# Performance work log

Measured on AMD Instinct MI355X. Metric: run time of the kernel, lower is better.

## Reference

```python
import jax, jax.numpy as jnp
import numpy as np
import math

D_MODEL = 1024
N_HEADS = 16
HEAD_DIM = D_MODEL // N_HEADS
B, S = 2, 2048


def setup_inputs() -> dict:
    key = jax.random.key(0)
    ks = jax.random.split(key, 12)
    sd = 1.0 / math.sqrt(D_MODEL)
    inp = {
        "x": jax.random.normal(ks[0], (B, S, D_MODEL), dtype=jnp.float32),
        "time_gaps": jax.random.uniform(ks[1], (B, S, 1), dtype=jnp.float32),
        "mask": jnp.ones((B, S), dtype=jnp.int32),
        "Wq": jax.random.normal(ks[2], (D_MODEL, D_MODEL), dtype=jnp.float32) * sd,
        "bq": jnp.zeros((D_MODEL,), dtype=jnp.float32),
        "Wk": jax.random.normal(ks[3], (D_MODEL, D_MODEL), dtype=jnp.float32) * sd,
        "bk": jnp.zeros((D_MODEL,), dtype=jnp.float32),
        "Wv": jax.random.normal(ks[4], (D_MODEL, D_MODEL), dtype=jnp.float32) * sd,
        "bv": jnp.zeros((D_MODEL,), dtype=jnp.float32),
        "Wo": jax.random.normal(ks[5], (D_MODEL, D_MODEL), dtype=jnp.float32) * sd,
        "bo": jnp.zeros((D_MODEL,), dtype=jnp.float32),
        "Wt": jax.random.normal(ks[6], (D_MODEL, 1), dtype=jnp.float32),
        "bt": jnp.zeros((D_MODEL,), dtype=jnp.float32),
    }
    return inp


def reference(x, time_gaps, mask, Wq, bq, Wk, bk, Wv, bv, Wo, bo, Wt, bt):
    Bb, Ss, _ = x.shape
    # time embedding: Linear(1, d_model)
    time_emb = time_gaps @ Wt.T + bt            # [B,S,D]
    x_time = x + time_emb

    def split_heads(t):
        return t.reshape(Bb, Ss, N_HEADS, HEAD_DIM).transpose(0, 2, 1, 3)  # [B,H,S,d]

    q = split_heads(x_time @ Wq.T + bq)
    k = split_heads(x_time @ Wk.T + bk)
    v = split_heads(x @ Wv.T + bv)

    scores = jnp.einsum('bhqd,bhkd->bhqk', q, k) / math.sqrt(HEAD_DIM)
    # padding mask: mask==0 positions set to -1e9 (mask broadcast as [B,1,1,S])
    pad = (mask == 0)[:, None, None, :]
    scores = jnp.where(pad, -1e9, scores)
    # causal mask
    causal = jnp.triu(jnp.ones((Ss, Ss), dtype=bool), k=1)
    scores = jnp.where(causal, -1e9, scores)

    attn = jax.nn.softmax(scores, axis=-1)      # dropout is identity in eval
    out = jnp.einsum('bhqk,bhkd->bhqd', attn, v)
    out = out.transpose(0, 2, 1, 3).reshape(Bb, Ss, D_MODEL)
    return out @ Wo.T + bo
```

## Files before the change

### kernel.cpp

```cpp
#include <hip/hip_runtime.h>

typedef short v8s __attribute__((ext_vector_type(8)));
typedef short v4s __attribute__((ext_vector_type(4)));
typedef float v4f __attribute__((ext_vector_type(4)));
typedef int   v4i __attribute__((ext_vector_type(4)));

constexpr int Bb = 2, S = 2048, D = 1024, H = 16;
constexpr int M = Bb * S;

#define DEV __device__ __forceinline__

DEV short f2bf(float f){
  unsigned u = __builtin_bit_cast(unsigned, f);
  u = (u + 0x7FFF + ((u >> 16) & 1)) >> 16;
  return (short)u;
}

DEV int swz(int r){ return (r ^ (r >> 2)) & 7; }

DEV int cvtpk(float lo, float hi){
  int r;
  asm("v_cvt_pk_bf16_f32 %0, %1, %2" : "=v"(r) : "v"(lo), "v"(hi));
  return r;
}

DEV float max3f(float a, float b, float c){
  float r;
  asm("v_max3_f32 %0, %1, %2, %3" : "=v"(r) : "v"(a), "v"(b), "v"(c));
  return r;
}

#define EXP2 exp2f

#define GLDS(gp, lp) __builtin_amdgcn_global_load_lds( \
    (const __attribute__((address_space(1))) void*)(gp), \
    (__attribute__((address_space(3))) void*)(lp), 16, 0, 0)

struct PrepArgs {
  const float* x; const float* tg; const float* Wt; const float* bt;
  const float* Ws0; const float* Ws1; const float* Ws2; const float* Ws3;
  short* Wd0; short* Wd1; short* Wd2; short* Wd3;
  short* xb; short* xtb;
};
__global__ void prep_all(PrepArgs a){
  const int bx = blockIdx.x;
  if (bx < 4096){
    int i = bx * 256 + threadIdx.x;
    int row = i >> 8;
    int c4  = i & 255;
    float4 xv = reinterpret_cast<const float4*>(a.x)[i];
    float4 wv = reinterpret_cast<const float4*>(a.Wt)[c4];
    float4 bv = reinterpret_cast<const float4*>(a.bt)[c4];
    float g = a.tg[row];
    float xs[4] = {xv.x, xv.y, xv.z, xv.w};
    float ws[4] = {wv.x, wv.y, wv.z, wv.w};
    float bs[4] = {bv.x, bv.y, bv.z, bv.w};
    v4s p, q;
    #pragma unroll
    for (int e = 0; e < 4; ++e){
      p[e] = f2bf(xs[e]);
      q[e] = f2bf(xs[e] + g * ws[e] + bs[e]);
    }
    *reinterpret_cast<v4s*>(&a.xb[(size_t)i * 4])  = p;
    *reinterpret_cast<v4s*>(&a.xtb[(size_t)i * 4]) = q;
  } else {
    const int bi = bx - 4096;
    const int widx = bi >> 10;
    const float* src = widx == 0 ? a.Ws0 : widx == 1 ? a.Ws1 : widx == 2 ? a.Ws2 : a.Ws3;
    short* dst = widx == 0 ? a.Wd0 : widx == 1 ? a.Wd1 : widx == 2 ? a.Wd2 : a.Wd3;
    int i = (bi & 1023) * 256 + threadIdx.x;
    float4 v = reinterpret_cast<const float4*>(src)[i];
    v4s o; o[0] = f2bf(v.x); o[1] = f2bf(v.y); o[2] = f2bf(v.z); o[3] = f2bf(v.w);
    *reinterpret_cast<v4s*>(&dst[(size_t)i * 4]) = o;
  }
}

template<int MODE>
DEV void gemm_core(const short* __restrict__ A, const short* __restrict__ Bw,
                   const float* __restrict__ bias, float alpha, void* __restrict__ Cout,
                   int ldc, int m0, int n0){
  __shared__ short As[2][128 * 64];
  __shared__ short Bs[2][128 * 64];
  const int t = threadIdx.x;
  const int w = t >> 6, l = t & 63;
  const int wm = (w >> 1) * 64, wn = (w & 1) * 64;

  v4f acc[4][4] = {};

  auto stage = [&](int kt, int buf){
    const int k0 = kt * 64;
    #pragma unroll
    for (int j = 0; j < 4; ++j){
      const int cix = j * 256 + t;
      const int row = cix >> 3;
      const int c   = (cix & 7) ^ swz(row);
      GLDS(A  + (size_t)(m0 + row) * D + k0 + c * 8, &As[buf][cix * 8]);
      GLDS(Bw + (size_t)(n0 + row) * D + k0 + c * 8, &Bs[buf][cix * 8]);
    }
  };

  stage(0, 0);
  for (int kt = 0; kt < 16; ++kt){
    const int cur = kt & 1;
    __syncthreads();
    if (kt < 15) stage(kt + 1, cur ^ 1);
    #pragma unroll
    for (int kk = 0; kk < 2; ++kk){
      v8s af[4], bfr[4];
      #pragma unroll
      for (int mi = 0; mi < 4; ++mi){
        const int R = wm + mi * 16 + (l & 15);
        af[mi] = *reinterpret_cast<const v8s*>(&As[cur][R * 64 + (((kk * 4 + (l >> 4)) ^ swz(R)) * 8)]);
      }
      #pragma unroll
      for (int ni = 0; ni < 4; ++ni){
        const int R = wn + ni * 16 + (l & 15);
        bfr[ni] = *reinterpret_cast<const v8s*>(&Bs[cur][R * 64 + (((kk * 4 + (l >> 4)) ^ swz(R)) * 8)]);
      }
      __builtin_amdgcn_s_setprio(1);
      #pragma unroll
      for (int mi = 0; mi < 4; ++mi)
        #pragma unroll
        for (int ni = 0; ni < 4; ++ni)
          acc[mi][ni] = __builtin_amdgcn_mfma_f32_16x16x32_bf16(af[mi], bfr[ni], acc[mi][ni], 0, 0, 0);
      __builtin_amdgcn_s_setprio(0);
    }
  }

  #pragma unroll
  for (int mi = 0; mi < 4; ++mi){
    const int row = m0 + wm + mi * 16 + (l >> 4) * 4;
    #pragma unroll
    for (int ni = 0; ni < 4; ++ni){
      const int col = n0 + wn + ni * 16 + (l & 15);
      const float bcol = (MODE == 1) ? 0.f : bias[col];
      #pragma unroll
      for (int r = 0; r < 4; ++r){
        float bsel = (MODE == 1) ? bias[row + r] : bcol;
        float val = (acc[mi][ni][r] + bsel) * alpha;
        if (MODE == 2) reinterpret_cast<float*>(Cout)[(size_t)(row + r) * ldc + col] = val;
        else           reinterpret_cast<short*>(Cout)[(size_t)(row + r) * ldc + col] = f2bf(val);
      }
    }
  }
}

template<int MODE>
__global__ __launch_bounds__(256, 2)
void gemm_bt(const short* __restrict__ A, const short* __restrict__ Bw,
             const float* __restrict__ bias, float alpha, void* __restrict__ Cout, int ldc){
  gemm_core<MODE>(A, Bw, bias, alpha, Cout, ldc, blockIdx.x * 128, blockIdx.y * 128);
}

__global__ __launch_bounds__(256, 2)
void gemm_qk(const short* __restrict__ A, const short* __restrict__ Wq,
             const short* __restrict__ Wk, const float* __restrict__ bq,
             const float* __restrict__ bk, float qalpha,
             short* __restrict__ Qb, short* __restrict__ Kb){
  const bool isK = blockIdx.y >= 8;
  gemm_core<0>(A, isK ? Wk : Wq, isK ? bk : bq, isK ? 1.0f : qalpha,
               isK ? (void*)Kb : (void*)Qb, D, blockIdx.x * 128, (blockIdx.y & 7) * 128);
}

__global__ __launch_bounds__(256, 3)
void attn_kernel(const short* __restrict__ Q, const short* __restrict__ K,
                 const short* __restrict__ VT, const int* __restrict__ maskp,
                 short* __restrict__ O){
  __shared__ short Ks[3][64 * 64];
  __shared__ short Vs[3][64 * 64];
  __shared__ int mflag;
  const int t = threadIdx.x, w = t >> 6, l = t & 63;
  const int g = l >> 4, q16 = l & 15;
  const int bh = blockIdx.x, b = bh >> 4, h = bh & 15;
  const int qx = 31 - (int)blockIdx.y;
  const int q0 = qx * 64;
  const int qw = q0 + w * 16;
  const int qg = qw + q16;
  const int nkt = qx + 1;

  if (t == 0) mflag = 1;
  __syncthreads();
  {
    bool ok = true;
    const int tot = nkt * 64;
    for (int i = t * 4; i < tot; i += 1024){
      v4i mm = *reinterpret_cast<const v4i*>(&maskp[b * S + i]);
      ok = ok && (mm[0] != 0) && (mm[1] != 0) && (mm[2] != 0) && (mm[3] != 0);
    }
    if (!__all(ok)) mflag = 0;
  }
  __syncthreads();
  const bool ALLV = (mflag != 0);

  v8s qf[2];
  #pragma unroll
  for (int kc = 0; kc < 2; ++kc)
    qf[kc] = *reinterpret_cast<const v8s*>(
        &Q[(size_t)(b * S + qg) * D + h * 64 + kc * 32 + g * 8]);

  int kOff[4][2], vOff[4][2];
  #pragma unroll
  for (int nt = 0; nt < 4; ++nt){
    const int R = 32 * (nt >> 1) + 8 * (q16 >> 2) + 4 * (nt & 1) + (l & 3);
    #pragma unroll
    for (int kc = 0; kc < 2; ++kc)
      kOff[nt][kc] = R * 64 + (((kc * 4 + g) ^ swz(R)) * 8);
  }
  #pragma unroll
  for (int dt = 0; dt < 4; ++dt){
    const int R = dt * 16 + q16;
    #pragma unroll
    for (int kc = 0; kc < 2; ++kc)
      vOff[dt][kc] = R * 64 + (((kc * 4 + g) ^ swz(R)) * 8);
  }

  v4f accOT[4] = {};
  v4f accL = {};
  float mrow = -1e30f;

  const v4i onesW = {0x3F803F80, 0x3F803F80, 0x3F803F80, 0x3F803F80};
  const v8s onesv = __builtin_bit_cast(v8s, onesW);

  auto stage = [&](int kt){
    const int buf = kt % 3;
    const int kv0 = kt * 64;
    #pragma unroll
    for (int j = 0; j < 2; ++j){
      const int cix = j * 256 + t;
      const int row = cix >> 3;
      const int c   = (cix & 7) ^ swz(row);
      GLDS(K  + (size_t)(b * S + kv0 + row) * D + h * 64 + c * 8, &Ks[buf][cix * 8]);
      GLDS(VT + (size_t)(h * 64 + row) * M + b * S + kv0 + c * 8, &Vs[buf][cix * 8]);
    }
  };

  auto softmax_pv = [&](float (&p)[16], const short* vb){
    float t0 = max3f(p[0], p[1], p[2]);
    float t1 = max3f(p[3], p[4], p[5]);
    float t2 = max3f(p[6], p[7], p[8]);
    float t3 = max3f(p[9], p[10], p[11]);
    float t4 = max3f(p[12], p[13], p[14]);
    float tm = max3f(max3f(t0, t1, t2), t3, fmaxf(t4, p[15]));
    if (!__all(tm <= mrow + 8.0f)){
      float tmax = fmaxf(tm, __shfl_xor(tm, 16));
      tmax = fmaxf(tmax, __shfl_xor(tmax, 32));
      const float mnew = fmaxf(mrow, tmax);
      const float resc = EXP2(mrow - mnew);
      #pragma unroll
      for (int dt = 0; dt < 4; ++dt) accOT[dt] *= resc;
      accL *= resc;
      mrow = mnew;
    }
    #pragma unroll
    for (int j = 0; j < 16; ++j) p[j] = EXP2(p[j] - mrow);

    int pb[2][4];
    #pragma unroll
    for (int kc = 0; kc < 2; ++kc)
      #pragma unroll
      for (int s = 0; s < 4; ++s){
        const int base = (2 * kc + (s >> 1)) * 4 + (s & 1) * 2;
        pb[kc][s] = cvtpk(p[base], p[base + 1]);
      }

    __builtin_amdgcn_s_setprio(1);
    #pragma unroll
    for (int kc = 0; kc < 2; ++kc){
      v4i tmp = {pb[kc][0], pb[kc][1], pb[kc][2], pb[kc][3]};
      v8s pbv = __builtin_bit_cast(v8s, tmp);
      accL = __builtin_amdgcn_mfma_f32_16x16x32_bf16(onesv, pbv, accL, 0, 0, 0);
      #pragma unroll
      for (int dt = 0; dt < 4; ++dt){
        v8s vf = *reinterpret_cast<const v8s*>(vb + vOff[dt][kc]);
        accOT[dt] = __builtin_amdgcn_mfma_f32_16x16x32_bf16(vf, pbv, accOT[dt], 0, 0, 0);
      }
    }
    __builtin_amdgcn_s_setprio(0);
  };

  auto qk = [&](const short* kb, v4f (&sc)[4]){
    __builtin_amdgcn_s_setprio(1);
    #pragma unroll
    for (int nt = 0; nt < 4; ++nt)
      #pragma unroll
      for (int kc = 0; kc < 2; ++kc){
        v8s kf = *reinterpret_cast<const v8s*>(kb + kOff[nt][kc]);
        sc[nt] = __builtin_amdgcn_mfma_f32_16x16x32_bf16(kf, qf[kc], sc[nt], 0, 0, 0);
      }
    __builtin_amdgcn_s_setprio(0);
  };

  stage(0);
  if (nkt > 1) stage(1);

  if (ALLV){
    for (int kt = 0; kt < nkt; ++kt){
      if (kt + 1 < nkt) asm volatile("s_waitcnt vmcnt(4)" ::: "memory");
      else              asm volatile("s_waitcnt vmcnt(0)" ::: "memory");
      __builtin_amdgcn_s_barrier();
      if (kt + 2 < nkt) stage(kt + 2);

      const int buf = kt % 3;
      const short* kb = Ks[buf];
      const short* vb = Vs[buf];

      v4f sc[4] = {};
      qk(kb, sc);

      float p[16];
      if (kt < qx){
        #pragma unroll
        for (int j = 0; j < 16; ++j) p[j] = sc[j >> 2][j & 3];
      } else {
        const int kv0 = kt * 64;
        #pragma unroll
        for (int nt = 0; nt < 4; ++nt)
          #pragma unroll
          for (int r = 0; r < 4; ++r){
            const int kvg = kv0 + 32 * (nt >> 1) + 8 * g + 4 * (nt & 1) + r;
            p[nt * 4 + r] = (kvg > qg) ? -1e30f : sc[nt][r];
          }
      }
      softmax_pv(p, vb);
    }
  } else {
    for (int kt = 0; kt < nkt; ++kt){
      asm volatile("s_waitcnt vmcnt(0)" ::: "memory");
      __builtin_amdgcn_s_barrier();
      if (kt + 2 < nkt) stage(kt + 2);

      const int buf = kt % 3;
      const short* kb = Ks[buf];
      const short* vb = Vs[buf];
      const int kv0 = kt * 64;

      v4i mq[4];
      #pragma unroll
      for (int nt = 0; nt < 4; ++nt)
        mq[nt] = *reinterpret_cast<const v4i*>(
            &maskp[b * S + kv0 + 32 * (nt >> 1) + 8 * g + 4 * (nt & 1)]);

      v4f sc[4] = {};
      qk(kb, sc);

      float p[16];
      #pragma unroll
      for (int nt = 0; nt < 4; ++nt)
        #pragma unroll
        for (int r = 0; r < 4; ++r){
          const int kvg = kv0 + 32 * (nt >> 1) + 8 * g + 4 * (nt & 1) + r;
          const int kvx = (mq[nt][r] != 0) ? kvg : 0x7fffffff;
          p[nt * 4 + r] = (kvx > qg) ? -1e30f : sc[nt][r];
        }
      softmax_pv(p, vb);
    }
  }

  const float inv = 1.0f / accL[0];
  #pragma unroll
  for (int dt = 0; dt < 4; ++dt){
    v4s o4;
    #pragma unroll
    for (int r = 0; r < 4; ++r) o4[r] = f2bf(accOT[dt][r] * inv);
    *reinterpret_cast<v4s*>(
        &O[(size_t)(b * S + qg) * D + h * 64 + dt * 16 + g * 4]) = o4;
  }
}

extern "C" void kernel_launch(void* const* d_in, const int* in_sizes, int n_in,
                              void* d_out, int out_size, void* d_ws, size_t ws_size,
                              hipStream_t stream){
  const float* x   = (const float*)d_in[0];
  const float* tg  = (const float*)d_in[1];
  const int*   msk = (const int*)d_in[2];
  const float* Wq  = (const float*)d_in[3];
  const float* bq  = (const float*)d_in[4];
  const float* Wk  = (const float*)d_in[5];
  const float* bk  = (const float*)d_in[6];
  const float* Wv  = (const float*)d_in[7];
  const float* bv  = (const float*)d_in[8];
  const float* Wo  = (const float*)d_in[9];
  const float* bo  = (const float*)d_in[10];
  const float* Wt  = (const float*)d_in[11];
  const float* bt  = (const float*)d_in[12];

  char* ws = (char*)d_ws;
  const size_t MB = 1u << 20;
  short* xb  = (short*)(ws);
  short* xtb = (short*)(ws + 8 * MB);
  short* Wqb = (short*)(ws + 16 * MB);
  short* Wkb = (short*)(ws + 18 * MB);
  short* Wvb = (short*)(ws + 20 * MB);
  short* Wob = (short*)(ws + 22 * MB);
  short* Qb  = (short*)(ws + 24 * MB);
  short* Kb  = (short*)(ws + 32 * MB);
  short* VTb = (short*)(ws + 40 * MB);
  short* Ab  = (short*)(ws + 48 * MB);

  PrepArgs pa;
  pa.x = x; pa.tg = tg; pa.Wt = Wt; pa.bt = bt;
  pa.Ws0 = Wq; pa.Ws1 = Wk; pa.Ws2 = Wv; pa.Ws3 = Wo;
  pa.Wd0 = Wqb; pa.Wd1 = Wkb; pa.Wd2 = Wvb; pa.Wd3 = Wob;
  pa.xb = xb; pa.xtb = xtb;
  prep_all<<<8192, 256, 0, stream>>>(pa);

  const float qalpha = 0.125f * 1.4426950408889634f;
  gemm_qk<<<dim3(M / 128, 16), 256, 0, stream>>>(xtb, Wqb, Wkb, bq, bk, qalpha, Qb, Kb);
  gemm_bt<1><<<dim3(D / 128, M / 128), 256, 0, stream>>>(Wvb, xb, bv, 1.0f, VTb, M);

  attn_kernel<<<dim3(Bb * H, 32), 256, 0, stream>>>(Qb, Kb, VTb, msk, Ab);

  gemm_bt<2><<<dim3(M / 128, D / 128), 256, 0, stream>>>(Ab, Wob, bo, 1.0f, (float*)d_out, D);
}
```

Baseline: 117.4 us.

## Fuse Q/K/V projections into one launch and double-buffer attention for occupancy

Merges the QK projection GEMM and the transposed V projection GEMM into a single 768-block launch, removing one kernel launch and the tail between them. The attention kernel drops from triple to double buffering of K/V tiles, which cuts LDS use so launch bounds can rise to 4 blocks per CU. It also remaps query-block order so heavy and light causal tiles interleave. The cost is a shallower prefetch: every iteration now waits for all outstanding loads, so global-load latency is hidden less.

```diff
diff --git a/kernel.cpp b/kernel.cpp
--- a/kernel.cpp
+++ b/kernel.cpp
@@ -153,26 +153,37 @@
 }
 
 __global__ __launch_bounds__(256, 2)
-void gemm_qk(const short* __restrict__ A, const short* __restrict__ Wq,
-             const short* __restrict__ Wk, const float* __restrict__ bq,
-             const float* __restrict__ bk, float qalpha,
-             short* __restrict__ Qb, short* __restrict__ Kb){
-  const bool isK = blockIdx.y >= 8;
-  gemm_core<0>(A, isK ? Wk : Wq, isK ? bk : bq, isK ? 1.0f : qalpha,
-               isK ? (void*)Kb : (void*)Qb, D, blockIdx.x * 128, (blockIdx.y & 7) * 128);
-}
-
-__global__ __launch_bounds__(256, 3)
+void gemm_qkv(const short* __restrict__ xtb, const short* __restrict__ xb,
+              const short* __restrict__ Wqb, const short* __restrict__ Wkb,
+              const short* __restrict__ Wvb,
+              const float* __restrict__ bq, const float* __restrict__ bk,
+              const float* __restrict__ bv, float qalpha,
+              short* __restrict__ Qb, short* __restrict__ Kb, short* __restrict__ VTb){
+  const int id = blockIdx.x;
+  if (id < 512){
+    const int li = id;
+    const int yq = li >> 5;
+    const bool isK = yq >= 8;
+    gemm_core<0>(xtb, isK ? Wkb : Wqb, isK ? bk : bq, isK ? 1.0f : qalpha,
+                 isK ? (void*)Kb : (void*)Qb, D, (li & 31) * 128, (yq & 7) * 128);
+  } else {
+    const int li = id - 512;
+    gemm_core<1>(Wvb, xb, bv, 1.0f, VTb, M, (li & 7) * 128, (li >> 3) * 128);
+  }
+}
+
+__global__ __launch_bounds__(256, 4)
 void attn_kernel(const short* __restrict__ Q, const short* __restrict__ K,
                  const short* __restrict__ VT, const int* __restrict__ maskp,
                  short* __restrict__ O){
-  __shared__ short Ks[3][64 * 64];
-  __shared__ short Vs[3][64 * 64];
+  __shared__ short Ks[2][64 * 64];
+  __shared__ short Vs[2][64 * 64];
   __shared__ int mflag;
   const int t = threadIdx.x, w = t >> 6, l = t & 63;
   const int g = l >> 4, q16 = l & 15;
   const int bh = blockIdx.x, b = bh >> 4, h = bh & 15;
-  const int qx = 31 - (int)blockIdx.y;
+  const int yy = (int)blockIdx.y;
+  const int qx = (yy < 8) ? 31 - yy : (yy < 16) ? yy - 8 : (yy < 24) ? 39 - yy : yy - 16;
   const int q0 = qx * 64;
   const int qw = q0 + w * 16;
   const int qg = qw + q16;
@@ -222,7 +233,7 @@
   const v8s onesv = __builtin_bit_cast(v8s, onesW);
 
   auto stage = [&](int kt){
-    const int buf = kt % 3;
+    const int buf = kt & 1;
     const int kv0 = kt * 64;
     #pragma unroll
     for (int j = 0; j < 2; ++j){
@@ -291,18 +302,15 @@
   };
 
   stage(0);
-  if (nkt > 1) stage(1);
 
   if (ALLV){
     for (int kt = 0; kt < nkt; ++kt){
-      if (kt + 1 < nkt) asm volatile("s_waitcnt vmcnt(4)" ::: "memory");
-      else              asm volatile("s_waitcnt vmcnt(0)" ::: "memory");
+      asm volatile("s_waitcnt vmcnt(0)" ::: "memory");
       __builtin_amdgcn_s_barrier();
-      if (kt + 2 < nkt) stage(kt + 2);
-
-      const int buf = kt % 3;
-      const short* kb = Ks[buf];
-      const short* vb = Vs[buf];
+      if (kt + 1 < nkt) stage(kt + 1);
+
+      const short* kb = Ks[kt & 1];
+      const short* vb = Vs[kt & 1];
 
       v4f sc[4] = {};
       qk(kb, sc);
@@ -327,11 +335,10 @@
     for (int kt = 0; kt < nkt; ++kt){
       asm volatile("s_waitcnt vmcnt(0)" ::: "memory");
       __builtin_amdgcn_s_barrier();
-      if (kt + 2 < nkt) stage(kt + 2);
-
-      const int buf = kt % 3;
-      const short* kb = Ks[buf];
-      const short* vb = Vs[buf];
+      if (kt + 1 < nkt) stage(kt + 1);
+
+      const short* kb = Ks[kt & 1];
+      const short* vb = Vs[kt & 1];
       const int kv0 = kt * 64;
 
       v4i mq[4];
@@ -405,8 +412,8 @@
   prep_all<<<8192, 256, 0, stream>>>(pa);
 
   const float qalpha = 0.125f * 1.4426950408889634f;
-  gemm_qk<<<dim3(M / 128, 16), 256, 0, stream>>>(xtb, Wqb, Wkb, bq, bk, qalpha, Qb, Kb);
-  gemm_bt<1><<<dim3(D / 128, M / 128), 256, 0, stream>>>(Wvb, xb, bv, 1.0f, VTb, M);
+  gemm_qkv<<<768, 256, 0, stream>>>(xtb, xb, Wqb, Wkb, Wvb, bq, bk, bv, qalpha,
+                                    Qb, Kb, VTb);
 
   attn_kernel<<<dim3(Bb * H, 32), 256, 0, stream>>>(Qb, Kb, VTb, msk, Ab);
 
```

New measurement: 139.3 us. 18.7% more time.
